# Performance work log

Measured on AMD Instinct MI355X. Metric: run time of the kernel, lower is better.

## Reference

```python
import jax, jax.numpy as jnp
import numpy as np

N_NODES = 50000
N_EDGES = 1600000
IN_CH = 128
HID = 128  # 2 * out_channels
NUM_GRAPHS = 64


def gcn_conv(x, row, col, ew, W, b, num_nodes):
    # PyG GCNConv: add self-loops (weight 1), symmetric degree norm, x @ W,
    # gather at source row, scale by norm, scatter-add at target col, add bias.
    loop = jnp.arange(num_nodes)
    r = jnp.concatenate([row, loop])
    c = jnp.concatenate([col, loop])
    w = jnp.concatenate([ew, jnp.ones((num_nodes,), ew.dtype)])
    deg = jax.ops.segment_sum(w, c, num_segments=num_nodes)
    dis = jnp.where(deg > 0, jax.lax.rsqrt(jnp.where(deg > 0, deg, 1.0)), 0.0)
    norm = dis[r] * w * dis[c]  # [E+N]
    xw = x @ W  # [N, HID]
    msg = xw[r] * norm[:, None]  # [E+N, HID] gather + scale
    out = jax.ops.segment_sum(msg, c, num_segments=num_nodes)
    return out + b


def setup_inputs() -> dict:
    key = jax.random.key(0)
    ks = jax.random.split(key, 8)
    x = jax.random.normal(ks[0], (N_NODES, IN_CH), dtype=jnp.float32)
    edge_index = jax.random.randint(ks[1], (2, N_EDGES), 0, N_NODES, dtype=jnp.int64)
    edge_weight = jax.random.uniform(ks[2], (N_EDGES,), dtype=jnp.float32)
    batch = jnp.sort(jax.random.randint(ks[3], (N_NODES,), 0, NUM_GRAPHS, dtype=jnp.int64))
    W1 = jax.random.normal(ks[4], (IN_CH, HID), dtype=jnp.float32) * 0.01
    b1 = jnp.zeros((HID,), jnp.float32)
    W2 = jax.random.normal(ks[5], (HID, HID), dtype=jnp.float32) * 0.01
    b2 = jnp.zeros((HID,), jnp.float32)
    return {"x": x, "edge_index": edge_index, "edge_weight": edge_weight,
            "batch": batch, "W1": W1, "b1": b1, "W2": W2, "b2": b2}


def reference(x, edge_index, edge_weight, batch, W1, b1, W2, b2):
    row, col = edge_index[0], edge_index[1]
    h = jax.nn.relu(gcn_conv(x, row, col, edge_weight, W1, b1, N_NODES))
    h = jax.nn.relu(gcn_conv(h, row, col, edge_weight, W2, b2, N_NODES))
    # global_mean_pool over batch segment ids
    sums = jax.ops.segment_sum(h, batch, num_segments=NUM_GRAPHS)
    cnts = jax.ops.segment_sum(jnp.ones((N_NODES,), h.dtype), batch, num_segments=NUM_GRAPHS)
    pooled = sums / jnp.maximum(cnts, 1.0)[:, None]
    return h, pooled
```

## Files before the change

### kernel.cpp

```cpp
#include <hip/hip_runtime.h>
#include <hip/hip_fp16.h>


#define CH 128
#define BSH 7
#define NBLK 1024
#define MAXNB 512
#define PCH 32
#define LDW 136

typedef __attribute__((ext_vector_type(8))) short bf16x8;
typedef __attribute__((ext_vector_type(4))) float f32x4;

static __device__ __forceinline__ unsigned short f2bf(float f) {
    unsigned u = __float_as_uint(f);
    unsigned r = (u + 0x7FFF + ((u >> 16) & 1)) >> 16;
    return (unsigned short)r;
}
static __device__ __forceinline__ float bflo(unsigned v) { return __uint_as_float(v << 16); }
static __device__ __forceinline__ float bfhi(unsigned v) { return __uint_as_float(v & 0xFFFF0000u); }
static __device__ __forceinline__ float f16u(unsigned bits15) {
    __half_raw hr; hr.x = (unsigned short)(bits15 & 0x7FFF);
    return __half2float(*reinterpret_cast<__half*>(&hr));
}
static __device__ __forceinline__ unsigned u16f(float f) {
    __half hh = __float2half(f);
    return (unsigned)(*reinterpret_cast<unsigned short*>(&hh)) & 0x7FFF;
}

__global__ __launch_bounds__(256) void k_sort1a(const int* __restrict__ col,
                                                int* __restrict__ H, int E, int NB, int chunk) {
    __shared__ int hist[MAXNB];
    int t = threadIdx.x, blk = blockIdx.x;
    for (int i = t; i < NB; i += 256) hist[i] = 0;
    __syncthreads();
    int s = blk * chunk, e1 = min(s + chunk, E);
    for (int e = s + t; e < e1; e += 256) atomicAdd(&hist[col[e] >> BSH], 1);
    __syncthreads();
    for (int i = t; i < NB; i += 256) H[(size_t)i * NBLK + blk] = hist[i];
}

__global__ __launch_bounds__(1024) void k_scan1(int* __restrict__ data,
                                                int* __restrict__ bsum, int n) {
    __shared__ int sd[1024];
    int t = threadIdx.x;
    int i = blockIdx.x * 1024 + t;
    int v = (i < n) ? data[i] : 0;
    sd[t] = v;
    __syncthreads();
    for (int off = 1; off < 1024; off <<= 1) {
        int u = (t >= off) ? sd[t - off] : 0;
        __syncthreads();
        sd[t] += u;
        __syncthreads();
    }
    if (i < n) data[i] = sd[t] - v;
    if (t == 1023) bsum[blockIdx.x] = sd[1023];
}

__global__ __launch_bounds__(1024) void k_scan2(int* bsum, int nb, int* total) {
    __shared__ int sd[1024];
    int t = threadIdx.x;
    int v = (t < nb) ? bsum[t] : 0;
    sd[t] = v;
    __syncthreads();
    for (int off = 1; off < 1024; off <<= 1) {
        int u = (t >= off) ? sd[t - off] : 0;
        __syncthreads();
        sd[t] += u;
        __syncthreads();
    }
    if (t < nb) bsum[t] = sd[t] - v;
    if (t == 1023) *total = sd[1023];
}

__global__ __launch_bounds__(256) void k_sort1b(const int* __restrict__ row,
                                                const int* __restrict__ col,
                                                const float* __restrict__ ew,
                                                const int* __restrict__ Hs,
                                                const int* __restrict__ bsum,
                                                int2* __restrict__ pairs2,
                                                int E, int NB, int chunk) {
    __shared__ int cur[MAXNB];
    int t = threadIdx.x, blk = blockIdx.x;
    for (int i = t; i < NB; i += 256) cur[i] = Hs[(size_t)i * NBLK + blk] + bsum[i];
    __syncthreads();
    int s = blk * chunk, e1 = min(s + chunk, E);
    for (int e = s + t; e < e1; e += 256) {
        int c = col[e];
        int pos = atomicAdd(&cur[c >> BSH], 1);
        pairs2[pos] = make_int2(row[e] | ((c & 127) << 17), __float_as_int(ew[e]));
    }
}

__global__ __launch_bounds__(256) void k_sort2(const int* __restrict__ Hs,
                                               const int* __restrict__ bsum,
                                               const int2* __restrict__ pairs2,
                                               unsigned* __restrict__ epk,
                                               int* __restrict__ rowptr,
                                               float* __restrict__ dis,
                                               int E, int N, int NB) {
    __shared__ int hist[128];
    __shared__ int pref[128];
    __shared__ float wsum[128];
    int b = blockIdx.x, t = threadIdx.x;
    int n0 = b << BSH;
    int s = Hs[(size_t)b * NBLK] + bsum[b];
    int e1 = (b + 1 < NB) ? Hs[(size_t)(b + 1) * NBLK] + bsum[b + 1] : E;
    if (t < 128) { hist[t] = 0; wsum[t] = 0.f; }
    __syncthreads();
    for (int e = s + t; e < e1; e += 256)
        atomicAdd(&hist[(unsigned)pairs2[e].x >> 17], 1);
    __syncthreads();
    if (t < 128) pref[t] = hist[t];
    __syncthreads();
    for (int off = 1; off < 128; off <<= 1) {
        int v = 0;
        if (t < 128 && t >= off) v = pref[t - off];
        __syncthreads();
        if (t < 128) pref[t] += v;
        __syncthreads();
    }
    if (t < 128) {
        int excl = pref[t] - hist[t];
        int node = n0 + t;
        if (node < N) rowptr[node] = s + excl;
        hist[t] = s + excl;
    }
    if (b == NB - 1 && t == 0) rowptr[N] = E;
    __syncthreads();
    for (int e = s + t; e < e1; e += 256) {
        int2 pr = pairs2[e];
        int li = (unsigned)pr.x >> 17;
        float w = __int_as_float(pr.y);
        int pos = atomicAdd(&hist[li], 1);
        epk[pos] = (unsigned)(pr.x & 0x1FFFF) | (u16f(w) << 17);
        atomicAdd(&wsum[li], w);
    }
    __syncthreads();
    if (t < 128 && n0 + t < N) dis[n0 + t] = rsqrtf(1.0f + wsum[t]);
}

__global__ __launch_bounds__(64) void k_norm(const int* __restrict__ rowptr,
                                             unsigned* __restrict__ epk,
                                             const float* __restrict__ dis, int N) {
    int n = blockIdx.x;
    int lane = threadIdx.x;
    float dn = dis[n];
    int e0 = rowptr[n], e1 = rowptr[n + 1];
    for (int e = e0 + lane; e < e1; e += 64) {
        unsigned v = epk[e];
        unsigned src = v & 0x1FFFF;
        float nn = dn * f16u(v >> 17) * dis[src];
        epk[e] = src | (u16f(nn) << 17);
    }
}

__global__ __launch_bounds__(512) void k_gemm(const float* __restrict__ X,
                                              const float* __restrict__ W,
                                              unsigned short* __restrict__ Y, int N) {
    __shared__ unsigned short Wt[128 * LDW];
    int tid = threadIdx.x;
    for (int i = tid; i < 4096; i += 512) {
        float4 v = ((const float4*)W)[i];
        int k = i >> 5;
        int c = (i & 31) * 4;
        Wt[(c + 0) * LDW + k] = f2bf(v.x);
        Wt[(c + 1) * LDW + k] = f2bf(v.y);
        Wt[(c + 2) * LDW + k] = f2bf(v.z);
        Wt[(c + 3) * LDW + k] = f2bf(v.w);
    }
    __syncthreads();
    int w = tid >> 6, lane = tid & 63;
    int l15 = lane & 15, kg = lane >> 4;
    int r = blockIdx.x * 128 + w * 16 + l15;
    f32x4 acc[8];
#pragma unroll
    for (int ct = 0; ct < 8; ++ct) acc[ct] = (f32x4){0.f, 0.f, 0.f, 0.f};
#pragma unroll
    for (int kb = 0; kb < 128; kb += 32) {
        union { unsigned u[4]; bf16x8 v; } a;
        if (r < N) {
            const float4* xp = (const float4*)(X + (size_t)r * CH + kb + kg * 8);
            float4 x0 = xp[0], x1 = xp[1];
            a.u[0] = ((unsigned)f2bf(x0.y) << 16) | f2bf(x0.x);
            a.u[1] = ((unsigned)f2bf(x0.w) << 16) | f2bf(x0.z);
            a.u[2] = ((unsigned)f2bf(x1.y) << 16) | f2bf(x1.x);
            a.u[3] = ((unsigned)f2bf(x1.w) << 16) | f2bf(x1.z);
        } else {
            a.u[0] = a.u[1] = a.u[2] = a.u[3] = 0;
        }
#pragma unroll
        for (int ct = 0; ct < 8; ++ct) {
            bf16x8 b = *(const bf16x8*)&Wt[(ct * 16 + l15) * LDW + kb + kg * 8];
            acc[ct] = __builtin_amdgcn_mfma_f32_16x16x32_bf16(a.v, b, acc[ct], 0, 0, 0);
        }
    }
    int orow = blockIdx.x * 128 + w * 16 + kg * 4;
#pragma unroll
    for (int ct = 0; ct < 8; ++ct) {
#pragma unroll
        for (int j = 0; j < 4; ++j) {
            int rr = orow + j;
            if (rr < N) Y[(size_t)rr * CH + ct * 16 + l15] = f2bf(acc[ct][j]);
        }
    }
}

__global__ __launch_bounds__(64) void k_agg(const unsigned int* __restrict__ XW,
                                            const float* __restrict__ dis,
                                            const int* __restrict__ rowptr,
                                            const unsigned* __restrict__ epk,
                                            const float* __restrict__ bias,
                                            float* __restrict__ OUT, int N) {
    int n = blockIdx.x;
    if (n >= N) return;
    int lane = threadIdx.x;
    float dn = dis[n];
    float sn = dn * dn;
    unsigned a = XW[(size_t)n * 64 + lane];
    float ax = bflo(a) * sn;
    float ay = bfhi(a) * sn;
    int e0 = rowptr[n], e1 = rowptr[n + 1];
    int e = e0;
    for (; e + 8 <= e1; e += 8) {
        unsigned p0 = epk[e],     p1 = epk[e + 1], p2 = epk[e + 2], p3 = epk[e + 3];
        unsigned p4 = epk[e + 4], p5 = epk[e + 5], p6 = epk[e + 6], p7 = epk[e + 7];
        unsigned v0 = XW[(size_t)(p0 & 0x1FFFF) * 64 + lane];
        unsigned v1 = XW[(size_t)(p1 & 0x1FFFF) * 64 + lane];
        unsigned v2 = XW[(size_t)(p2 & 0x1FFFF) * 64 + lane];
        unsigned v3 = XW[(size_t)(p3 & 0x1FFFF) * 64 + lane];
        unsigned v4 = XW[(size_t)(p4 & 0x1FFFF) * 64 + lane];
        unsigned v5 = XW[(size_t)(p5 & 0x1FFFF) * 64 + lane];
        unsigned v6 = XW[(size_t)(p6 & 0x1FFFF) * 64 + lane];
        unsigned v7 = XW[(size_t)(p7 & 0x1FFFF) * 64 + lane];
        float n0 = f16u(p0 >> 17), n1 = f16u(p1 >> 17);
        float n2 = f16u(p2 >> 17), n3 = f16u(p3 >> 17);
        float n4 = f16u(p4 >> 17), n5 = f16u(p5 >> 17);
        float n6 = f16u(p6 >> 17), n7 = f16u(p7 >> 17);
        ax += n0 * bflo(v0) + n1 * bflo(v1) + n2 * bflo(v2) + n3 * bflo(v3)
            + n4 * bflo(v4) + n5 * bflo(v5) + n6 * bflo(v6) + n7 * bflo(v7);
        ay += n0 * bfhi(v0) + n1 * bfhi(v1) + n2 * bfhi(v2) + n3 * bfhi(v3)
            + n4 * bfhi(v4) + n5 * bfhi(v5) + n6 * bfhi(v6) + n7 * bfhi(v7);
    }
    for (; e < e1; ++e) {
        unsigned p = epk[e];
        unsigned v = XW[(size_t)(p & 0x1FFFF) * 64 + lane];
        float nn = f16u(p >> 17);
        ax += nn * bflo(v);
        ay += nn * bfhi(v);
    }
    float2 b = ((const float2*)bias)[lane];
    ax = fmaxf(ax + b.x, 0.f);
    ay = fmaxf(ay + b.y, 0.f);
    ((float2*)OUT)[(size_t)n * 64 + lane] = make_float2(ax, ay);
}

__device__ __forceinline__ int lowerb(const int* a, int n, int v) {
    int lo = 0, hi = n;
    while (lo < hi) {
        int m = (lo + hi) >> 1;
        if (a[m] < v) lo = m + 1; else hi = m;
    }
    return lo;
}

__global__ __launch_bounds__(128) void k_pool1(const float* __restrict__ H,
                                               const int* __restrict__ batch,
                                               float* __restrict__ partial, int N) {
    __shared__ int ss[2];
    int g = blockIdx.x / PCH;
    int k = blockIdx.x % PCH;
    if (threadIdx.x == 0) {
        ss[0] = lowerb(batch, N, g);
        ss[1] = lowerb(batch, N, g + 1);
    }
    __syncthreads();
    int s = ss[0], len = ss[1] - ss[0];
    int cs = s + (int)(((long long)len * k) / PCH);
    int ce = s + (int)(((long long)len * (k + 1)) / PCH);
    int ch = threadIdx.x;
    float a0 = 0.f, a1 = 0.f;
    int n = cs;
    for (; n + 2 <= ce; n += 2) {
        a0 += H[(size_t)(n + 0) * CH + ch];
        a1 += H[(size_t)(n + 1) * CH + ch];
    }
    for (; n < ce; ++n) a0 += H[(size_t)n * CH + ch];
    partial[(size_t)blockIdx.x * CH + ch] = a0 + a1;
}

__global__ __launch_bounds__(128) void k_pool2(const float* __restrict__ partial,
                                               const int* __restrict__ batch,
                                               float* __restrict__ P, int N) {
    __shared__ int ss[2];
    int g = blockIdx.x;
    if (threadIdx.x == 0) {
        ss[0] = lowerb(batch, N, g);
        ss[1] = lowerb(batch, N, g + 1);
    }
    __syncthreads();
    int ch = threadIdx.x;
    float a = 0.f;
#pragma unroll
    for (int k = 0; k < PCH; ++k) a += partial[(size_t)(g * PCH + k) * CH + ch];
    float c = (float)(ss[1] - ss[0]);
    P[(size_t)g * CH + ch] = a / fmaxf(c, 1.f);
}

extern "C" void kernel_launch(void* const* d_in, const int* in_sizes, int n_in,
                              void* d_out, int out_size, void* d_ws, size_t ws_size,
                              hipStream_t stream) {
    const float* x     = (const float*)d_in[0];
    const int*   ei    = (const int*)d_in[1];
    const float* ew    = (const float*)d_in[2];
    const int*   batch = (const int*)d_in[3];
    const float* W1    = (const float*)d_in[4];
    const float* b1    = (const float*)d_in[5];
    const float* W2    = (const float*)d_in[6];
    const float* b2    = (const float*)d_in[7];

    int N = in_sizes[0] / CH;
    int E = in_sizes[1] / 2;
    const int* row = ei;
    const int* col = ei + E;

    float* out    = (float*)d_out;
    float* h      = out;
    float* pooled = out + (size_t)N * CH;

    int NB    = (N + 127) >> BSH;
    int chunk = (E + NBLK - 1) / NBLK;
    int n2    = NB * NBLK;

    char* wsb = (char*)d_ws;
    size_t oN  = ((size_t)N * 4 + 255) & ~(size_t)255;
    size_t oN1 = ((size_t)(N + 1) * 4 + 255) & ~(size_t)255;
    size_t oH  = ((size_t)(n2 + 1) * 4 + 255) & ~(size_t)255;
    size_t oB  = 4096;
    size_t oE1 = ((size_t)E * 4 + 255) & ~(size_t)255;
    float* dis    = (float*)wsb;
    int*   rowptr = (int*)(wsb + oN);
    int*   H      = (int*)(wsb + oN + oN1);
    int*   bsum   = (int*)(wsb + oN + oN1 + oH);
    unsigned* epk = (unsigned*)(wsb + oN + oN1 + oH + oB);
    unsigned short* xw = (unsigned short*)(wsb + oN + oN1 + oH + oB + oE1);
    int2*  pairs2 = (int2*)xw;
    float* partial = (float*)H;

    int sb2 = (n2 + 1023) / 1024;

    k_sort1a<<<NBLK, 256, 0, stream>>>(col, H, E, NB, chunk);
    k_scan1<<<sb2, 1024, 0, stream>>>(H, bsum, n2);
    k_scan2<<<1, 1024, 0, stream>>>(bsum, sb2, H + n2);
    k_sort1b<<<NBLK, 256, 0, stream>>>(row, col, ew, H, bsum, pairs2, E, NB, chunk);
    k_sort2<<<NB, 256, 0, stream>>>(H, bsum, pairs2, epk, rowptr, dis, E, N, NB);
    k_norm<<<N, 64, 0, stream>>>(rowptr, epk, dis, N);

    int gb = (N + 127) / 128;
    k_gemm<<<gb, 512, 0, stream>>>(x, W1, xw, N);
    k_agg<<<N, 64, 0, stream>>>((const unsigned int*)xw, dis, rowptr, epk, b1, h, N);
    k_gemm<<<gb, 512, 0, stream>>>(h, W2, xw, N);
    k_agg<<<N, 64, 0, stream>>>((const unsigned int*)xw, dis, rowptr, epk, b2, h, N);
    k_pool1<<<64 * PCH, 128, 0, stream>>>(h, batch, partial, N);
    k_pool2<<<64, 128, 0, stream>>>(partial, batch, pooled, N);
}
```

Measured before the change: 223.7 us.

## Split XW into column halves for cache-resident aggregation and fuse scan kernels

The GEMM now writes XW in a column-split layout: two planes of 64 bf16 columns each. Aggregation runs as two passes, one per half, so each pass gathers from a 6.4MB table that fits better in cache. Each wave handles one node, with its two half-waves taking alternate edges and combining through a shuffle; edge and output accesses use nontemporal loads and stores. Separately, the second scan kernel is merged into the first with a last-block atomic counter, removing one launch at the cost of reading the edge list twice per layer.

Result: slower. 343.2 us (+53.4%).

```diff
diff --git a/kernel.cpp b/kernel.cpp
--- a/kernel.cpp
+++ b/kernel.cpp
@@ -11,6 +11,7 @@
 
 typedef __attribute__((ext_vector_type(8))) short bf16x8;
 typedef __attribute__((ext_vector_type(4))) float f32x4;
+typedef __attribute__((ext_vector_type(2))) float f32x2;
 
 static __device__ __forceinline__ unsigned short f2bf(float f) {
     unsigned u = __float_as_uint(f);
@@ -29,9 +30,11 @@
 }
 
 __global__ __launch_bounds__(256) void k_sort1a(const int* __restrict__ col,
-                                                int* __restrict__ H, int E, int NB, int chunk) {
+                                                int* __restrict__ H, int* __restrict__ cnt,
+                                                int E, int NB, int chunk) {
     __shared__ int hist[MAXNB];
     int t = threadIdx.x, blk = blockIdx.x;
+    if (blk == 0 && t == 0) *cnt = 0;
     for (int i = t; i < NB; i += 256) hist[i] = 0;
     __syncthreads();
     int s = blk * chunk, e1 = min(s + chunk, E);
@@ -41,8 +44,10 @@
 }
 
 __global__ __launch_bounds__(1024) void k_scan1(int* __restrict__ data,
-                                                int* __restrict__ bsum, int n) {
+                                                int* __restrict__ bsum,
+                                                int* __restrict__ cnt, int n, int nb) {
     __shared__ int sd[1024];
+    __shared__ int lastFlag;
     int t = threadIdx.x;
     int i = blockIdx.x * 1024 + t;
     int v = (i < n) ? data[i] : 0;
@@ -55,23 +60,25 @@
         __syncthreads();
     }
     if (i < n) data[i] = sd[t] - v;
-    if (t == 1023) bsum[blockIdx.x] = sd[1023];
-}
-
-__global__ __launch_bounds__(1024) void k_scan2(int* bsum, int nb, int* total) {
-    __shared__ int sd[1024];
-    int t = threadIdx.x;
-    int v = (t < nb) ? bsum[t] : 0;
-    sd[t] = v;
-    __syncthreads();
-    for (int off = 1; off < 1024; off <<= 1) {
-        int u = (t >= off) ? sd[t - off] : 0;
-        __syncthreads();
-        sd[t] += u;
-        __syncthreads();
-    }
-    if (t < nb) bsum[t] = sd[t] - v;
-    if (t == 1023) *total = sd[1023];
+    if (t == 1023) {
+        bsum[blockIdx.x] = sd[1023];
+        __threadfence();
+        lastFlag = (atomicAdd(cnt, 1) == (int)gridDim.x - 1);
+    }
+    __syncthreads();
+    if (lastFlag) {
+        __threadfence();
+        int v2 = (t < nb) ? bsum[t] : 0;
+        sd[t] = v2;
+        __syncthreads();
+        for (int off = 1; off < 1024; off <<= 1) {
+            int u = (t >= off) ? sd[t - off] : 0;
+            __syncthreads();
+            sd[t] += u;
+            __syncthreads();
+        }
+        if (t < nb) bsum[t] = sd[t] - v2;
+    }
 }
 
 __global__ __launch_bounds__(256) void k_sort1b(const int* __restrict__ row,
@@ -199,41 +206,47 @@
     int orow = blockIdx.x * 128 + w * 16 + kg * 4;
 #pragma unroll
     for (int ct = 0; ct < 8; ++ct) {
+        int c = ct * 16 + l15;
+        unsigned short* Yb = Y + (size_t)(c >> 6) * N * 64 + (c & 63);
 #pragma unroll
         for (int j = 0; j < 4; ++j) {
             int rr = orow + j;
-            if (rr < N) Y[(size_t)rr * CH + ct * 16 + l15] = f2bf(acc[ct][j]);
+            if (rr < N) Yb[(size_t)rr * 64] = f2bf(acc[ct][j]);
         }
     }
 }
 
-__global__ __launch_bounds__(64) void k_agg(const unsigned int* __restrict__ XW,
-                                            const float* __restrict__ dis,
-                                            const int* __restrict__ rowptr,
-                                            const unsigned* __restrict__ epk,
-                                            const float* __restrict__ bias,
-                                            float* __restrict__ OUT, int N) {
-    int n = blockIdx.x;
+__global__ __launch_bounds__(256) void k_aggc(const unsigned* __restrict__ XWC,
+                                              const float* __restrict__ dis,
+                                              const int* __restrict__ rowptr,
+                                              const unsigned* __restrict__ epk,
+                                              const float* __restrict__ bias,
+                                              float* __restrict__ OUT,
+                                              int col0, int N) {
+    int n = blockIdx.x * 4 + (threadIdx.x >> 6);
     if (n >= N) return;
-    int lane = threadIdx.x;
-    float dn = dis[n];
-    float sn = dn * dn;
-    unsigned a = XW[(size_t)n * 64 + lane];
-    float ax = bflo(a) * sn;
-    float ay = bfhi(a) * sn;
+    int lane = threadIdx.x & 63;
+    int g = lane >> 5, li = lane & 31;
+    float ax = 0.f, ay = 0.f;
     int e0 = rowptr[n], e1 = rowptr[n + 1];
-    int e = e0;
-    for (; e + 8 <= e1; e += 8) {
-        unsigned p0 = epk[e],     p1 = epk[e + 1], p2 = epk[e + 2], p3 = epk[e + 3];
-        unsigned p4 = epk[e + 4], p5 = epk[e + 5], p6 = epk[e + 6], p7 = epk[e + 7];
-        unsigned v0 = XW[(size_t)(p0 & 0x1FFFF) * 64 + lane];
-        unsigned v1 = XW[(size_t)(p1 & 0x1FFFF) * 64 + lane];
-        unsigned v2 = XW[(size_t)(p2 & 0x1FFFF) * 64 + lane];
-        unsigned v3 = XW[(size_t)(p3 & 0x1FFFF) * 64 + lane];
-        unsigned v4 = XW[(size_t)(p4 & 0x1FFFF) * 64 + lane];
-        unsigned v5 = XW[(size_t)(p5 & 0x1FFFF) * 64 + lane];
-        unsigned v6 = XW[(size_t)(p6 & 0x1FFFF) * 64 + lane];
-        unsigned v7 = XW[(size_t)(p7 & 0x1FFFF) * 64 + lane];
+    int e = e0 + g;
+    for (; e + 14 < e1; e += 16) {
+        unsigned p0 = __builtin_nontemporal_load(&epk[e]);
+        unsigned p1 = __builtin_nontemporal_load(&epk[e + 2]);
+        unsigned p2 = __builtin_nontemporal_load(&epk[e + 4]);
+        unsigned p3 = __builtin_nontemporal_load(&epk[e + 6]);
+        unsigned p4 = __builtin_nontemporal_load(&epk[e + 8]);
+        unsigned p5 = __builtin_nontemporal_load(&epk[e + 10]);
+        unsigned p6 = __builtin_nontemporal_load(&epk[e + 12]);
+        unsigned p7 = __builtin_nontemporal_load(&epk[e + 14]);
+        unsigned v0 = XWC[(size_t)(p0 & 0x1FFFF) * 32 + li];
+        unsigned v1 = XWC[(size_t)(p1 & 0x1FFFF) * 32 + li];
+        unsigned v2 = XWC[(size_t)(p2 & 0x1FFFF) * 32 + li];
+        unsigned v3 = XWC[(size_t)(p3 & 0x1FFFF) * 32 + li];
+        unsigned v4 = XWC[(size_t)(p4 & 0x1FFFF) * 32 + li];
+        unsigned v5 = XWC[(size_t)(p5 & 0x1FFFF) * 32 + li];
+        unsigned v6 = XWC[(size_t)(p6 & 0x1FFFF) * 32 + li];
+        unsigned v7 = XWC[(size_t)(p7 & 0x1FFFF) * 32 + li];
         float n0 = f16u(p0 >> 17), n1 = f16u(p1 >> 17);
         float n2 = f16u(p2 >> 17), n3 = f16u(p3 >> 17);
         float n4 = f16u(p4 >> 17), n5 = f16u(p5 >> 17);
@@ -243,17 +256,29 @@
         ay += n0 * bfhi(v0) + n1 * bfhi(v1) + n2 * bfhi(v2) + n3 * bfhi(v3)
             + n4 * bfhi(v4) + n5 * bfhi(v5) + n6 * bfhi(v6) + n7 * bfhi(v7);
     }
-    for (; e < e1; ++e) {
-        unsigned p = epk[e];
-        unsigned v = XW[(size_t)(p & 0x1FFFF) * 64 + lane];
+    for (; e < e1; e += 2) {
+        unsigned p = __builtin_nontemporal_load(&epk[e]);
+        unsigned v = XWC[(size_t)(p & 0x1FFFF) * 32 + li];
         float nn = f16u(p >> 17);
         ax += nn * bflo(v);
         ay += nn * bfhi(v);
     }
-    float2 b = ((const float2*)bias)[lane];
-    ax = fmaxf(ax + b.x, 0.f);
-    ay = fmaxf(ay + b.y, 0.f);
-    ((float2*)OUT)[(size_t)n * 64 + lane] = make_float2(ax, ay);
+    if (g == 0) {
+        float dn = dis[n];
+        float sn = dn * dn;
+        unsigned a = XWC[(size_t)n * 32 + li];
+        ax += sn * bflo(a);
+        ay += sn * bfhi(a);
+    }
+    ax += __shfl_xor(ax, 32);
+    ay += __shfl_xor(ay, 32);
+    if (g == 0) {
+        float2 b = *(const float2*)&bias[col0 + li * 2];
+        f32x2 o;
+        o.x = fmaxf(ax + b.x, 0.f);
+        o.y = fmaxf(ay + b.y, 0.f);
+        __builtin_nontemporal_store(o, (f32x2*)&OUT[(size_t)n * CH + col0 + li * 2]);
+    }
 }
 
 __device__ __forceinline__ int lowerb(const int* a, int n, int v) {
@@ -337,12 +362,13 @@
     size_t oN  = ((size_t)N * 4 + 255) & ~(size_t)255;
     size_t oN1 = ((size_t)(N + 1) * 4 + 255) & ~(size_t)255;
     size_t oH  = ((size_t)(n2 + 1) * 4 + 255) & ~(size_t)255;
-    size_t oB  = 4096;
+    size_t oB  = 8192;
     size_t oE1 = ((size_t)E * 4 + 255) & ~(size_t)255;
     float* dis    = (float*)wsb;
     int*   rowptr = (int*)(wsb + oN);
     int*   H      = (int*)(wsb + oN + oN1);
     int*   bsum   = (int*)(wsb + oN + oN1 + oH);
+    int*   cnt    = bsum + 1024;
     unsigned* epk = (unsigned*)(wsb + oN + oN1 + oH + oB);
     unsigned short* xw = (unsigned short*)(wsb + oN + oN1 + oH + oB + oE1);
     int2*  pairs2 = (int2*)xw;
@@ -350,18 +376,21 @@
 
     int sb2 = (n2 + 1023) / 1024;
 
-    k_sort1a<<<NBLK, 256, 0, stream>>>(col, H, E, NB, chunk);
-    k_scan1<<<sb2, 1024, 0, stream>>>(H, bsum, n2);
-    k_scan2<<<1, 1024, 0, stream>>>(bsum, sb2, H + n2);
+    k_sort1a<<<NBLK, 256, 0, stream>>>(col, H, cnt, E, NB, chunk);
+    k_scan1<<<sb2, 1024, 0, stream>>>(H, bsum, cnt, n2, sb2);
     k_sort1b<<<NBLK, 256, 0, stream>>>(row, col, ew, H, bsum, pairs2, E, NB, chunk);
     k_sort2<<<NB, 256, 0, stream>>>(H, bsum, pairs2, epk, rowptr, dis, E, N, NB);
     k_norm<<<N, 64, 0, stream>>>(rowptr, epk, dis, N);
 
     int gb = (N + 127) / 128;
+    int ab = (N + 3) / 4;
+    const unsigned* xw32 = (const unsigned*)xw;
     k_gemm<<<gb, 512, 0, stream>>>(x, W1, xw, N);
-    k_agg<<<N, 64, 0, stream>>>((const unsigned int*)xw, dis, rowptr, epk, b1, h, N);
+    k_aggc<<<ab, 256, 0, stream>>>(xw32, dis, rowptr, epk, b1, h, 0, N);
+    k_aggc<<<ab, 256, 0, stream>>>(xw32 + (size_t)N * 32, dis, rowptr, epk, b1, h, 64, N);
     k_gemm<<<gb, 512, 0, stream>>>(h, W2, xw, N);
-    k_agg<<<N, 64, 0, stream>>>((const unsigned int*)xw, dis, rowptr, epk, b2, h, N);
+    k_aggc<<<ab, 256, 0, stream>>>(xw32, dis, rowptr, epk, b2, h, 0, N);
+    k_aggc<<<ab, 256, 0, stream>>>(xw32 + (size_t)N * 32, dis, rowptr, epk, b2, h, 64, N);
     k_pool1<<<64 * PCH, 128, 0, stream>>>(h, batch, partial, N);
     k_pool2<<<64, 128, 0, stream>>>(partial, batch, pooled, N);
 }
```

## Fuse scan passes via last-block atomic and vectorize edge loads in aggregation

Applied to the files above, without the earlier changes.

Merges the second-level scan into the first scan kernel using a global atomic counter, so the last finishing block scans the block sums. This removes one kernel launch. The aggregation kernel now reads packed edges with 16-byte loads after an alignment prologue and unrolls to 16 gathers per iteration for more memory-level parallelism. Side effects: the total written at H+n2 is no longer produced, the fence-based last-block pattern is more complex, and register use in the aggregation kernel rises.

Result: slower. 233.7 us (+4.5%).

```diff
diff --git a/kernel.cpp b/kernel.cpp
--- a/kernel.cpp
+++ b/kernel.cpp
@@ -29,9 +29,11 @@
 }
 
 __global__ __launch_bounds__(256) void k_sort1a(const int* __restrict__ col,
-                                                int* __restrict__ H, int E, int NB, int chunk) {
+                                                int* __restrict__ H, int* __restrict__ cnt,
+                                                int E, int NB, int chunk) {
     __shared__ int hist[MAXNB];
     int t = threadIdx.x, blk = blockIdx.x;
+    if (blk == 0 && t == 0) *cnt = 0;
     for (int i = t; i < NB; i += 256) hist[i] = 0;
     __syncthreads();
     int s = blk * chunk, e1 = min(s + chunk, E);
@@ -41,8 +43,10 @@
 }
 
 __global__ __launch_bounds__(1024) void k_scan1(int* __restrict__ data,
-                                                int* __restrict__ bsum, int n) {
+                                                int* __restrict__ bsum,
+                                                int* __restrict__ cnt, int n, int nb) {
     __shared__ int sd[1024];
+    __shared__ int lastFlag;
     int t = threadIdx.x;
     int i = blockIdx.x * 1024 + t;
     int v = (i < n) ? data[i] : 0;
@@ -55,23 +59,25 @@
         __syncthreads();
     }
     if (i < n) data[i] = sd[t] - v;
-    if (t == 1023) bsum[blockIdx.x] = sd[1023];
-}
-
-__global__ __launch_bounds__(1024) void k_scan2(int* bsum, int nb, int* total) {
-    __shared__ int sd[1024];
-    int t = threadIdx.x;
-    int v = (t < nb) ? bsum[t] : 0;
-    sd[t] = v;
-    __syncthreads();
-    for (int off = 1; off < 1024; off <<= 1) {
-        int u = (t >= off) ? sd[t - off] : 0;
-        __syncthreads();
-        sd[t] += u;
-        __syncthreads();
-    }
-    if (t < nb) bsum[t] = sd[t] - v;
-    if (t == 1023) *total = sd[1023];
+    if (t == 1023) {
+        bsum[blockIdx.x] = sd[1023];
+        __threadfence();
+        lastFlag = (atomicAdd(cnt, 1) == (int)gridDim.x - 1);
+    }
+    __syncthreads();
+    if (lastFlag) {
+        __threadfence();
+        int v2 = (t < nb) ? bsum[t] : 0;
+        sd[t] = v2;
+        __syncthreads();
+        for (int off = 1; off < 1024; off <<= 1) {
+            int u = (t >= off) ? sd[t - off] : 0;
+            __syncthreads();
+            sd[t] += u;
+            __syncthreads();
+        }
+        if (t < nb) bsum[t] = sd[t] - v2;
+    }
 }
 
 __global__ __launch_bounds__(256) void k_sort1b(const int* __restrict__ row,
@@ -207,6 +213,14 @@
     }
 }
 
+#define GATHER(p) XW[(size_t)((p) & 0x1FFFF) * 64 + lane]
+#define ACC4(q, va, vb, vc, vd)                                           \
+    {                                                                     \
+        float na = f16u((q).x >> 17), nb = f16u((q).y >> 17);             \
+        float nc = f16u((q).z >> 17), nd = f16u((q).w >> 17);             \
+        ax += na * bflo(va) + nb * bflo(vb) + nc * bflo(vc) + nd * bflo(vd); \
+        ay += na * bfhi(va) + nb * bfhi(vb) + nc * bfhi(vc) + nd * bfhi(vd); \
+    }
 __global__ __launch_bounds__(64) void k_agg(const unsigned int* __restrict__ XW,
                                             const float* __restrict__ dis,
                                             const int* __restrict__ rowptr,
@@ -223,29 +237,35 @@
     float ay = bfhi(a) * sn;
     int e0 = rowptr[n], e1 = rowptr[n + 1];
     int e = e0;
-    for (; e + 8 <= e1; e += 8) {
-        unsigned p0 = epk[e],     p1 = epk[e + 1], p2 = epk[e + 2], p3 = epk[e + 3];
-        unsigned p4 = epk[e + 4], p5 = epk[e + 5], p6 = epk[e + 6], p7 = epk[e + 7];
-        unsigned v0 = XW[(size_t)(p0 & 0x1FFFF) * 64 + lane];
-        unsigned v1 = XW[(size_t)(p1 & 0x1FFFF) * 64 + lane];
-        unsigned v2 = XW[(size_t)(p2 & 0x1FFFF) * 64 + lane];
-        unsigned v3 = XW[(size_t)(p3 & 0x1FFFF) * 64 + lane];
-        unsigned v4 = XW[(size_t)(p4 & 0x1FFFF) * 64 + lane];
-        unsigned v5 = XW[(size_t)(p5 & 0x1FFFF) * 64 + lane];
-        unsigned v6 = XW[(size_t)(p6 & 0x1FFFF) * 64 + lane];
-        unsigned v7 = XW[(size_t)(p7 & 0x1FFFF) * 64 + lane];
-        float n0 = f16u(p0 >> 17), n1 = f16u(p1 >> 17);
-        float n2 = f16u(p2 >> 17), n3 = f16u(p3 >> 17);
-        float n4 = f16u(p4 >> 17), n5 = f16u(p5 >> 17);
-        float n6 = f16u(p6 >> 17), n7 = f16u(p7 >> 17);
-        ax += n0 * bflo(v0) + n1 * bflo(v1) + n2 * bflo(v2) + n3 * bflo(v3)
-            + n4 * bflo(v4) + n5 * bflo(v5) + n6 * bflo(v6) + n7 * bflo(v7);
-        ay += n0 * bfhi(v0) + n1 * bfhi(v1) + n2 * bfhi(v2) + n3 * bfhi(v3)
-            + n4 * bfhi(v4) + n5 * bfhi(v5) + n6 * bfhi(v6) + n7 * bfhi(v7);
+    for (; e < e1 && (e & 3); ++e) {
+        unsigned p = epk[e];
+        unsigned v = GATHER(p);
+        float nn = f16u(p >> 17);
+        ax += nn * bflo(v);
+        ay += nn * bfhi(v);
+    }
+    for (; e + 16 <= e1; e += 16) {
+        uint4 q0 = *(const uint4*)&epk[e];
+        uint4 q1 = *(const uint4*)&epk[e + 4];
+        uint4 q2 = *(const uint4*)&epk[e + 8];
+        uint4 q3 = *(const uint4*)&epk[e + 12];
+        unsigned v0 = GATHER(q0.x), v1 = GATHER(q0.y), v2 = GATHER(q0.z), v3 = GATHER(q0.w);
+        unsigned v4 = GATHER(q1.x), v5 = GATHER(q1.y), v6 = GATHER(q1.z), v7 = GATHER(q1.w);
+        unsigned v8 = GATHER(q2.x), v9 = GATHER(q2.y), va = GATHER(q2.z), vb = GATHER(q2.w);
+        unsigned vc = GATHER(q3.x), vd = GATHER(q3.y), ve = GATHER(q3.z), vf = GATHER(q3.w);
+        ACC4(q0, v0, v1, v2, v3);
+        ACC4(q1, v4, v5, v6, v7);
+        ACC4(q2, v8, v9, va, vb);
+        ACC4(q3, vc, vd, ve, vf);
+    }
+    for (; e + 4 <= e1; e += 4) {
+        uint4 q = *(const uint4*)&epk[e];
+        unsigned v0 = GATHER(q.x), v1 = GATHER(q.y), v2 = GATHER(q.z), v3 = GATHER(q.w);
+        ACC4(q, v0, v1, v2, v3);
     }
     for (; e < e1; ++e) {
         unsigned p = epk[e];
-        unsigned v = XW[(size_t)(p & 0x1FFFF) * 64 + lane];
+        unsigned v = GATHER(p);
         float nn = f16u(p >> 17);
         ax += nn * bflo(v);
         ay += nn * bfhi(v);
@@ -337,12 +357,13 @@
     size_t oN  = ((size_t)N * 4 + 255) & ~(size_t)255;
     size_t oN1 = ((size_t)(N + 1) * 4 + 255) & ~(size_t)255;
     size_t oH  = ((size_t)(n2 + 1) * 4 + 255) & ~(size_t)255;
-    size_t oB  = 4096;
+    size_t oB  = 8192;
     size_t oE1 = ((size_t)E * 4 + 255) & ~(size_t)255;
     float* dis    = (float*)wsb;
     int*   rowptr = (int*)(wsb + oN);
     int*   H      = (int*)(wsb + oN + oN1);
     int*   bsum   = (int*)(wsb + oN + oN1 + oH);
+    int*   cnt    = bsum + 1024;
     unsigned* epk = (unsigned*)(wsb + oN + oN1 + oH + oB);
     unsigned short* xw = (unsigned short*)(wsb + oN + oN1 + oH + oB + oE1);
     int2*  pairs2 = (int2*)xw;
@@ -350,9 +371,8 @@
 
     int sb2 = (n2 + 1023) / 1024;
 
-    k_sort1a<<<NBLK, 256, 0, stream>>>(col, H, E, NB, chunk);
-    k_scan1<<<sb2, 1024, 0, stream>>>(H, bsum, n2);
-    k_scan2<<<1, 1024, 0, stream>>>(bsum, sb2, H + n2);
+    k_sort1a<<<NBLK, 256, 0, stream>>>(col, H, cnt, E, NB, chunk);
+    k_scan1<<<sb2, 1024, 0, stream>>>(H, bsum, cnt, n2, sb2);
     k_sort1b<<<NBLK, 256, 0, stream>>>(row, col, ew, H, bsum, pairs2, E, NB, chunk);
     k_sort2<<<NB, 256, 0, stream>>>(H, bsum, pairs2, epk, rowptr, dis, E, N, NB);
     k_norm<<<N, 64, 0, stream>>>(rowptr, epk, dis, N);
```
